# Optimization experiments

Hardware: AMD Instinct MI355X
Metric: run time of the kernel (lower is better)

The kernel has to match this reference:

```python
import jax, jax.numpy as jnp
import numpy as np

D = 512
M_FUT = 3
EPS = 1e-12


def _lin(x, W, b):
    return x @ W + b


def _svd_orthogonalize(m):
    # m: [B, 9] -> [B, 3, 3] SO(3) via SVD orthogonalization (special Procrustes)
    m = m.reshape(-1, 3, 3)
    norm = jnp.maximum(jnp.linalg.norm(m, axis=-1, keepdims=True), EPS)
    mt = jnp.swapaxes(m / norm, -1, -2)          # normalize rows, then transpose
    u, s, vh = jnp.linalg.svd(mt, full_matrices=False)
    v = jnp.swapaxes(vh, -1, -2)                 # torch.svd returns V, jax returns V^H
    ut = jnp.swapaxes(u, -1, -2)
    det = jnp.linalg.det(jnp.matmul(v, ut))      # [B]
    v_adj = jnp.concatenate([v[:, :, :-1], v[:, :, -1:] * det[:, None, None]], axis=2)
    return jnp.matmul(v_adj, ut)


def setup_inputs() -> dict:
    key = jax.random.key(0)
    ks = iter(jax.random.split(key, 40))
    B, N, M = 32, 3, M_FUT
    ph = pw = 37
    BN, hw = B * N, ph * pw
    sc = 1.0 / np.sqrt(D)
    rn = lambda *shape: (jax.random.normal(next(ks), shape, dtype=jnp.float32) * sc)
    inp = {
        'feat': jax.random.normal(next(ks), (BN, hw, D), dtype=jnp.float32),
        'patch_h': ph, 'patch_w': pw, 'batch_size': B, 'num_current_frames': N,
        # two ResConvBlocks, three 512x512 Linears each (in==out -> skip is identity)
        'W_res': rn(2, 3, D, D), 'b_res': rn(2, 3, D),
        # TemporalCameraMLP
        'W_cur1': rn(D, D), 'b_cur1': rn(D), 'W_cur2': rn(D, D), 'b_cur2': rn(D),
        'W_tp1': rn(D, D), 'b_tp1': rn(D), 'W_tp2': rn(D, D * M), 'b_tp2': rn(D * M),
        'W_fut1': rn(D, D), 'b_fut1': rn(D), 'W_fut2': rn(D, D), 'b_fut2': rn(D),
        # more_mlps
        'W_m1': rn(D, D), 'b_m1': rn(D), 'W_m2': rn(D, D), 'b_m2': rn(D),
        # pose heads (fp32)
        'W_t': rn(D, 3), 'b_t': rn(3), 'W_r': rn(D, 9), 'b_r': rn(9),
    }
    return inp


def reference(feat, patch_h, patch_w, batch_size, num_current_frames,
              W_res, b_res, W_cur1, b_cur1, W_cur2, b_cur2,
              W_tp1, b_tp1, W_tp2, b_tp2, W_fut1, b_fut1, W_fut2, b_fut2,
              W_m1, b_m1, W_m2, b_m2, W_t, b_t, W_r, b_r):
    B, N = batch_size, num_current_frames
    M = W_tp2.shape[1] // W_tp2.shape[0]
    # stacked residual 1x1-conv (Linear) blocks
    for i in range(2):
        x = jax.nn.relu(_lin(feat, W_res[i, 0], b_res[i, 0]))
        x = jax.nn.relu(_lin(x, W_res[i, 1], b_res[i, 1]))
        x = jax.nn.relu(_lin(x, W_res[i, 2], b_res[i, 2]))
        feat = feat + x
    # AdaptiveAvgPool2d(1) over patch grid == mean over hw
    pooled = feat.mean(axis=1)                                  # [BN, D]
    # TemporalCameraMLP
    cur = _lin(jax.nn.relu(_lin(pooled, W_cur1, b_cur1)), W_cur2, b_cur2)   # [BN, D]
    gctx = pooled.reshape(B, N, -1).mean(axis=1)                            # [B, D]
    tf = _lin(jax.nn.relu(_lin(gctx, W_tp1, b_tp1)), W_tp2, b_tp2)          # [B, D*M]
    tf = tf.reshape(B * M, -1)
    fut = _lin(jax.nn.relu(_lin(tf, W_fut1, b_fut1)), W_fut2, b_fut2)       # [B*M, D]
    allf = jnp.concatenate([cur, fut], axis=0)                              # [B*(N+M), D]
    h = jax.nn.relu(_lin(jax.nn.relu(_lin(allf, W_m1, b_m1)), W_m2, b_m2))
    # pose head in fp32
    hf = h.astype(jnp.float32)
    out_t = _lin(hf, W_t, b_t)                                  # [newBN, 3]
    out_r = _lin(hf, W_r, b_r)                                  # [newBN, 9]
    r = _svd_orthogonalize(out_r)                               # [newBN, 3, 3]
    newBN = allf.shape[0]
    pose = jnp.zeros((newBN, 4, 4), dtype=jnp.float32)
    pose = pose.at[:, :3, :3].set(r)
    pose = pose.at[:, :3, 3].set(out_t)
    pose = pose.at[:, 3, 3].set(1.0)
    return pose
```

## Files before the change

### kernel.cpp

```cpp
#include <hip/hip_runtime.h>


typedef unsigned short u16;
typedef __attribute__((ext_vector_type(8))) short short8;
typedef __attribute__((ext_vector_type(4))) float f32x4;

constexpr int  DDIM   = 512;
constexpr long R_ROWS = 96L * 1369L;
constexpr long R_PAD  = 1027L * 128L;

__device__ __forceinline__ u16 f2b(float f) {
  union { float f; unsigned u; } x; x.f = f;
  unsigned r = (x.u + 0x7FFFu + ((x.u >> 16) & 1u)) >> 16;
  return (u16)r;
}
__device__ __forceinline__ float b2f(u16 b) {
  union { unsigned u; float f; } x; x.u = ((unsigned)b) << 16;
  return x.f;
}

__global__ void convert_feat_k(const float* __restrict__ in, u16* __restrict__ out) {
  long i4 = ((long)blockIdx.x * 256 + threadIdx.x) * 4;
  if (i4 >= R_PAD * DDIM) return;
  ushort4 o;
  if (i4 < R_ROWS * DDIM) {
    float4 v = *(const float4*)(in + i4);
    o.x = f2b(v.x); o.y = f2b(v.y); o.z = f2b(v.z); o.w = f2b(v.w);
  } else {
    o.x = 0; o.y = 0; o.z = 0; o.w = 0;
  }
  *(ushort4*)(out + i4) = o;
}

__global__ void transpose_w_k(const float* __restrict__ W, u16* __restrict__ Wt) {
  int idx = blockIdx.x * 256 + threadIdx.x;
  if (idx >= 6 * 512 * 512) return;
  int g = idx >> 18, rem = idx & 262143;
  int n = rem >> 9, k = rem & 511;
  Wt[idx] = f2b(W[(long)g * 262144 + (long)k * 512 + n]);
}

template <int MODE>
__global__ __launch_bounds__(256, 2)
void gemm_k(const u16* __restrict__ X, const u16* __restrict__ Wt,
            const float* __restrict__ bias, const u16* Res, u16* Y) {
  __shared__ u16 lA[128 * 64];
  __shared__ u16 lB[128 * 64];
  const int tid  = threadIdx.x;
  const int lane = tid & 63;
  const int wv   = tid >> 6;
  const int wm   = wv & 1;
  const int wn   = wv >> 1;
  const int l15  = lane & 15;
  const int quad = lane >> 4;
  const int colBase = blockIdx.x * 128;
  const long rowBase = (long)blockIdx.y * 128;

  f32x4 acc[4][4];
#pragma unroll
  for (int i = 0; i < 4; ++i)
#pragma unroll
    for (int j = 0; j < 4; ++j) acc[i][j] = (f32x4){0.f, 0.f, 0.f, 0.f};

  for (int k0 = 0; k0 < 512; k0 += 64) {
#pragma unroll
    for (int j = 0; j < 4; ++j) {
      int chunk = tid + 256 * j;
      int r = chunk >> 3, c = chunk & 7;
      const u16* ga = X + (rowBase + r) * DDIM + (k0 + c * 8);
      __builtin_amdgcn_global_load_lds(
          (const __attribute__((address_space(1))) void*)ga,
          (__attribute__((address_space(3))) void*)&lA[chunk * 8], 16, 0, 0);
      const u16* gb = Wt + (long)(colBase + r) * DDIM + (k0 + c * 8);
      __builtin_amdgcn_global_load_lds(
          (const __attribute__((address_space(1))) void*)gb,
          (__attribute__((address_space(3))) void*)&lB[chunk * 8], 16, 0, 0);
    }
    __syncthreads();
#pragma unroll
    for (int kk = 0; kk < 2; ++kk) {
      short8 af[4], bf[4];
#pragma unroll
      for (int i = 0; i < 4; ++i)
        af[i] = *(const short8*)&lA[(wm * 64 + i * 16 + l15) * 64 + kk * 32 + quad * 8];
#pragma unroll
      for (int j = 0; j < 4; ++j)
        bf[j] = *(const short8*)&lB[(wn * 64 + j * 16 + l15) * 64 + kk * 32 + quad * 8];
#pragma unroll
      for (int i = 0; i < 4; ++i)
#pragma unroll
        for (int j = 0; j < 4; ++j)
          acc[i][j] = __builtin_amdgcn_mfma_f32_16x16x32_bf16(af[i], bf[j], acc[i][j], 0, 0, 0);
    }
    __syncthreads();
  }

#pragma unroll
  for (int j = 0; j < 4; ++j) {
    int col = colBase + wn * 64 + j * 16 + l15;
    float bv = bias[col];
#pragma unroll
    for (int i = 0; i < 4; ++i) {
      long row0 = rowBase + wm * 64 + i * 16 + quad * 4;
#pragma unroll
      for (int r = 0; r < 4; ++r) {
        float v = acc[i][j][r] + bv;
        v = fmaxf(v, 0.f);
        long idx = (row0 + r) * DDIM + col;
        if (MODE == 1) v += b2f(Res[idx]);
        Y[idx] = f2b(v);
      }
    }
  }
}

__global__ void zero_k(float* p, int n) {
  int i = blockIdx.x * 256 + threadIdx.x;
  if (i < n) p[i] = 0.f;
}

__global__ void pool_k(const u16* __restrict__ feat, float* __restrict__ pooled) {
  int bn = blockIdx.x, ch = blockIdx.y, d = threadIdx.x;
  int p0 = ch * 172, p1 = p0 + 172;
  if (p1 > 1369) p1 = 1369;
  float s = 0.f;
  long base = ((long)bn * 1369 + p0) * DDIM + d;
  for (int p = p0; p < p1; ++p) { s += b2f(feat[base]); base += DDIM; }
  atomicAdd(&pooled[bn * DDIM + d], s * (1.0f / 1369.0f));
}

__global__ void gctx_k(const float* __restrict__ pooled, float* __restrict__ gctx) {
  int i = blockIdx.x * 256 + threadIdx.x;
  if (i >= 32 * DDIM) return;
  int b = i >> 9, d = i & 511;
  const float* p = pooled + (long)b * 3 * DDIM + d;
  gctx[i] = (p[0] + p[DDIM] + p[2 * DDIM]) * (1.0f / 3.0f);
}

template <bool RELU>
__global__ void lin_k(const float* __restrict__ in, const float* __restrict__ W,
                      const float* __restrict__ bias, float* __restrict__ out,
                      int K, int N) {
  int n = blockIdx.x * 256 + threadIdx.x;
  int r = blockIdx.y;
  if (n >= N) return;
  float acc = bias[n];
  const float* xi = in + (long)r * K;
#pragma unroll 8
  for (int k = 0; k < K; ++k) acc = fmaf(xi[k], W[(long)k * N + n], acc);
  if (RELU) acc = fmaxf(acc, 0.f);
  out[(long)r * N + n] = acc;
}

__global__ void pose_k(const float* __restrict__ h,
                       const float* __restrict__ Wt, const float* __restrict__ bt,
                       const float* __restrict__ Wr, const float* __restrict__ br,
                       float* __restrict__ out) {
  int row = blockIdx.x;
  int lane = threadIdx.x;
  const float* hr = h + (long)row * DDIM;
  float part[12];
#pragma unroll
  for (int c = 0; c < 12; ++c) {
    float acc = 0.f;
    for (int k = lane; k < DDIM; k += 64) {
      float wvv = (c < 3) ? Wt[k * 3 + c] : Wr[k * 9 + (c - 3)];
      acc += hr[k] * wvv;
    }
#pragma unroll
    for (int off = 32; off > 0; off >>= 1) acc += __shfl_down(acc, off);
    part[c] = acc;
  }
  if (lane != 0) return;

  double t3[3];
  for (int i = 0; i < 3; ++i) t3[i] = (double)part[i] + (double)bt[i];
  double m[3][3];
  for (int i = 0; i < 3; ++i)
    for (int j = 0; j < 3; ++j) m[i][j] = (double)part[3 + i * 3 + j] + (double)br[i * 3 + j];
  for (int i = 0; i < 3; ++i) {
    double nn = sqrt(m[i][0] * m[i][0] + m[i][1] * m[i][1] + m[i][2] * m[i][2]);
    if (nn < 1e-12) nn = 1e-12;
    m[i][0] /= nn; m[i][1] /= nn; m[i][2] /= nn;
  }
  double Km[3][3];
  for (int a = 0; a < 3; ++a)
    for (int b = 0; b < 3; ++b) {
      double s = 0;
      for (int i = 0; i < 3; ++i) s += m[i][a] * m[i][b];
      Km[a][b] = s;
    }
  double V[3][3] = {{1, 0, 0}, {0, 1, 0}, {0, 0, 1}};
  const int PQ[3][2] = {{0, 1}, {0, 2}, {1, 2}};
  for (int sweep = 0; sweep < 20; ++sweep) {
    for (int e = 0; e < 3; ++e) {
      int p = PQ[e][0], q = PQ[e][1];
      double apq = Km[p][q];
      if (apq == 0.0) continue;
      double tau = (Km[q][q] - Km[p][p]) / (2.0 * apq);
      double tt = (tau >= 0.0 ? 1.0 : -1.0) / (fabs(tau) + sqrt(1.0 + tau * tau));
      double cc = 1.0 / sqrt(1.0 + tt * tt), ss = tt * cc;
      for (int k = 0; k < 3; ++k) { double a1 = Km[p][k], a2 = Km[q][k]; Km[p][k] = cc * a1 - ss * a2; Km[q][k] = ss * a1 + cc * a2; }
      for (int k = 0; k < 3; ++k) { double a1 = Km[k][p], a2 = Km[k][q]; Km[k][p] = cc * a1 - ss * a2; Km[k][q] = ss * a1 + cc * a2; }
      for (int k = 0; k < 3; ++k) { double a1 = V[k][p], a2 = V[k][q]; V[k][p] = cc * a1 - ss * a2; V[k][q] = ss * a1 + cc * a2; }
    }
  }
  double lam[3] = {Km[0][0], Km[1][1], Km[2][2]};
  int o0 = 0, o1 = 1, o2 = 2; double detV = 1.0;
  if (lam[o0] < lam[o1]) { int t = o0; o0 = o1; o1 = t; detV = -detV; }
  if (lam[o1] < lam[o2]) { int t = o1; o1 = o2; o2 = t; detV = -detV; }
  if (lam[o0] < lam[o1]) { int t = o0; o0 = o1; o1 = t; detV = -detV; }
  double v0[3] = {V[0][o0], V[1][o0], V[2][o0]};
  double v1[3] = {V[0][o1], V[1][o1], V[2][o1]};
  double v2[3] = {V[0][o2], V[1][o2], V[2][o2]};
  double u0[3], u1[3];
  for (int i = 0; i < 3; ++i) u0[i] = m[i][0] * v0[0] + m[i][1] * v0[1] + m[i][2] * v0[2];
  double n0 = sqrt(u0[0] * u0[0] + u0[1] * u0[1] + u0[2] * u0[2]); if (n0 < 1e-30) n0 = 1e-30;
  for (int i = 0; i < 3; ++i) u0[i] /= n0;
  for (int i = 0; i < 3; ++i) u1[i] = m[i][0] * v1[0] + m[i][1] * v1[1] + m[i][2] * v1[2];
  double d01 = u0[0] * u1[0] + u0[1] * u1[1] + u0[2] * u1[2];
  for (int i = 0; i < 3; ++i) u1[i] -= d01 * u0[i];
  double n1 = sqrt(u1[0] * u1[0] + u1[1] * u1[1] + u1[2] * u1[2]); if (n1 < 1e-30) n1 = 1e-30;
  for (int i = 0; i < 3; ++i) u1[i] /= n1;
  double u2[3] = {u0[1] * u1[2] - u0[2] * u1[1],
                  u0[2] * u1[0] - u0[0] * u1[2],
                  u0[0] * u1[1] - u0[1] * u1[0]};
  float* o = out + (long)row * 16;
  for (int i = 0; i < 3; ++i) {
    for (int j = 0; j < 3; ++j)
      o[i * 4 + j] = (float)(u0[i] * v0[j] + u1[i] * v1[j] + detV * u2[i] * v2[j]);
    o[i * 4 + 3] = (float)t3[i];
  }
  o[12] = 0.f; o[13] = 0.f; o[14] = 0.f; o[15] = 1.f;
}

extern "C" void kernel_launch(void* const* d_in, const int* in_sizes, int n_in,
                              void* d_out, int out_size, void* d_ws, size_t ws_size,
                              hipStream_t stream) {
  (void)in_sizes; (void)n_in; (void)out_size; (void)ws_size;
  const float* feat   = (const float*)d_in[0];
  const float* W_res  = (const float*)d_in[5];
  const float* b_res  = (const float*)d_in[6];
  const float* W_cur1 = (const float*)d_in[7];
  const float* b_cur1 = (const float*)d_in[8];
  const float* W_cur2 = (const float*)d_in[9];
  const float* b_cur2 = (const float*)d_in[10];
  const float* W_tp1  = (const float*)d_in[11];
  const float* b_tp1  = (const float*)d_in[12];
  const float* W_tp2  = (const float*)d_in[13];
  const float* b_tp2  = (const float*)d_in[14];
  const float* W_fut1 = (const float*)d_in[15];
  const float* b_fut1 = (const float*)d_in[16];
  const float* W_fut2 = (const float*)d_in[17];
  const float* b_fut2 = (const float*)d_in[18];
  const float* W_m1   = (const float*)d_in[19];
  const float* b_m1   = (const float*)d_in[20];
  const float* W_m2   = (const float*)d_in[21];
  const float* b_m2   = (const float*)d_in[22];
  const float* W_t    = (const float*)d_in[23];
  const float* b_t    = (const float*)d_in[24];
  const float* W_r    = (const float*)d_in[25];
  const float* b_r    = (const float*)d_in[26];

  char* ws = (char*)d_ws;
  const size_t SZ_BIG = (size_t)R_PAD * DDIM * 2;
  u16* A   = (u16*)(ws);
  u16* Bb  = (u16*)(ws + SZ_BIG);
  u16* Cb  = (u16*)(ws + 2 * SZ_BIG);
  u16* Wt6 = (u16*)(ws + 3 * SZ_BIG);
  char* tail = ws + 3 * SZ_BIG + (size_t)6 * 512 * 512 * 2;
  float* pooled = (float*)(tail);
  float* gctx   = pooled + 96 * 512;
  float* tmp    = gctx + 32 * 512;
  float* tfb    = tmp + 192 * 512;
  float* allf   = tfb + 32 * 1536;
  float* h2     = allf + 192 * 512;
  float* outp   = (float*)d_out;

  convert_feat_k<<<65728, 256, 0, stream>>>(feat, A);
  transpose_w_k<<<6144, 256, 0, stream>>>(W_res, Wt6);

  dim3 gg(4, 1027);
  const size_t WS1 = (size_t)512 * 512;
  gemm_k<0><<<gg, 256, 0, stream>>>(A,  Wt6 + 0 * WS1, b_res + 0 * 512, nullptr, Bb);
  gemm_k<0><<<gg, 256, 0, stream>>>(Bb, Wt6 + 1 * WS1, b_res + 1 * 512, nullptr, Cb);
  gemm_k<1><<<gg, 256, 0, stream>>>(Cb, Wt6 + 2 * WS1, b_res + 2 * 512, A, A);
  gemm_k<0><<<gg, 256, 0, stream>>>(A,  Wt6 + 3 * WS1, b_res + 3 * 512, nullptr, Bb);
  gemm_k<0><<<gg, 256, 0, stream>>>(Bb, Wt6 + 4 * WS1, b_res + 4 * 512, nullptr, Cb);
  gemm_k<1><<<gg, 256, 0, stream>>>(Cb, Wt6 + 5 * WS1, b_res + 5 * 512, A, A);

  zero_k<<<(96 * 512 + 255) / 256, 256, 0, stream>>>(pooled, 96 * 512);
  pool_k<<<dim3(96, 8), 512, 0, stream>>>(A, pooled);
  gctx_k<<<(32 * 512 + 255) / 256, 256, 0, stream>>>(pooled, gctx);

  lin_k<true ><<<dim3(2, 96),  256, 0, stream>>>(pooled, W_cur1, b_cur1, tmp, 512, 512);
  lin_k<false><<<dim3(2, 96),  256, 0, stream>>>(tmp, W_cur2, b_cur2, allf, 512, 512);
  lin_k<true ><<<dim3(2, 32),  256, 0, stream>>>(gctx, W_tp1, b_tp1, tmp, 512, 512);
  lin_k<false><<<dim3(6, 32),  256, 0, stream>>>(tmp, W_tp2, b_tp2, tfb, 512, 1536);
  lin_k<true ><<<dim3(2, 96),  256, 0, stream>>>(tfb, W_fut1, b_fut1, tmp, 512, 512);
  lin_k<false><<<dim3(2, 96),  256, 0, stream>>>(tmp, W_fut2, b_fut2, allf + 96 * 512, 512, 512);
  lin_k<true ><<<dim3(2, 192), 256, 0, stream>>>(allf, W_m1, b_m1, tmp, 512, 512);
  lin_k<true ><<<dim3(2, 192), 256, 0, stream>>>(tmp, W_m2, b_m2, h2, 512, 512);

  pose_k<<<192, 64, 0, stream>>>(h2, W_t, b_t, W_r, b_r, outp);
}
```

Before: 1.695 ms.

## Swizzle LDS tiles, group GEMM blocks by row window, raise occupancy

The GEMM kernel now stores A and B tiles in LDS with an XOR swizzle on the 16-byte chunk index. Reads apply the matching swizzle, which is meant to remove bank conflicts on the short8 fragment loads. The 2D grid becomes a 1D grid in which 8 row tiles × 4 column tiles are grouped together, so blocks running at the same time share A rows and weight columns in L2. Launch bounds go from 2 to 4 blocks per CU, which adds some padded blocks that exit early and puts pressure on the register budget.

```diff
diff --git a/kernel.cpp b/kernel.cpp
--- a/kernel.cpp
+++ b/kernel.cpp
@@ -5,9 +5,10 @@
 typedef __attribute__((ext_vector_type(8))) short short8;
 typedef __attribute__((ext_vector_type(4))) float f32x4;
 
-constexpr int  DDIM   = 512;
-constexpr long R_ROWS = 96L * 1369L;
-constexpr long R_PAD  = 1027L * 128L;
+constexpr int  DDIM    = 512;
+constexpr long R_ROWS  = 96L * 1369L;
+constexpr long R_PAD   = 1027L * 128L;
+constexpr int  RT_GRID = 1032;
 
 __device__ __forceinline__ u16 f2b(float f) {
   union { float f; unsigned u; } x; x.f = f;
@@ -41,7 +42,7 @@
 }
 
 template <int MODE>
-__global__ __launch_bounds__(256, 2)
+__global__ __launch_bounds__(256, 4)
 void gemm_k(const u16* __restrict__ X, const u16* __restrict__ Wt,
             const float* __restrict__ bias, const u16* Res, u16* Y) {
   __shared__ u16 lA[128 * 64];
@@ -53,8 +54,14 @@
   const int wn   = wv >> 1;
   const int l15  = lane & 15;
   const int quad = lane >> 4;
-  const int colBase = blockIdx.x * 128;
-  const long rowBase = (long)blockIdx.y * 128;
+
+  const int b   = blockIdx.x;
+  const int win = b >> 5, i32 = b & 31;
+  const int rt  = win * 8 + (i32 & 7);
+  const int ct  = i32 >> 3;
+  if (rt >= 1027) return;
+  const int  colBase = ct * 128;
+  const long rowBase = (long)rt * 128;
 
   f32x4 acc[4][4];
 #pragma unroll
@@ -65,32 +72,34 @@
   for (int k0 = 0; k0 < 512; k0 += 64) {
 #pragma unroll
     for (int j = 0; j < 4; ++j) {
-      int chunk = tid + 256 * j;
-      int r = chunk >> 3, c = chunk & 7;
+      int L = tid + 256 * j;
+      int r = L >> 3, cS = L & 7;
+      int c = cS ^ (r & 7);
       const u16* ga = X + (rowBase + r) * DDIM + (k0 + c * 8);
       __builtin_amdgcn_global_load_lds(
           (const __attribute__((address_space(1))) void*)ga,
-          (__attribute__((address_space(3))) void*)&lA[chunk * 8], 16, 0, 0);
+          (__attribute__((address_space(3))) void*)&lA[L * 8], 16, 0, 0);
       const u16* gb = Wt + (long)(colBase + r) * DDIM + (k0 + c * 8);
       __builtin_amdgcn_global_load_lds(
           (const __attribute__((address_space(1))) void*)gb,
-          (__attribute__((address_space(3))) void*)&lB[chunk * 8], 16, 0, 0);
+          (__attribute__((address_space(3))) void*)&lB[L * 8], 16, 0, 0);
     }
     __syncthreads();
 #pragma unroll
     for (int kk = 0; kk < 2; ++kk) {
-      short8 af[4], bf[4];
+      const int cx = (((kk * 4 + quad) ^ (l15 & 7))) * 8;
+      short8 af[4], bfr[4];
 #pragma unroll
       for (int i = 0; i < 4; ++i)
-        af[i] = *(const short8*)&lA[(wm * 64 + i * 16 + l15) * 64 + kk * 32 + quad * 8];
+        af[i] = *(const short8*)&lA[(wm * 64 + i * 16 + l15) * 64 + cx];
 #pragma unroll
       for (int j = 0; j < 4; ++j)
-        bf[j] = *(const short8*)&lB[(wn * 64 + j * 16 + l15) * 64 + kk * 32 + quad * 8];
+        bfr[j] = *(const short8*)&lB[(wn * 64 + j * 16 + l15) * 64 + cx];
 #pragma unroll
       for (int i = 0; i < 4; ++i)
 #pragma unroll
         for (int j = 0; j < 4; ++j)
-          acc[i][j] = __builtin_amdgcn_mfma_f32_16x16x32_bf16(af[i], bf[j], acc[i][j], 0, 0, 0);
+          acc[i][j] = __builtin_amdgcn_mfma_f32_16x16x32_bf16(af[i], bfr[j], acc[i][j], 0, 0, 0);
     }
     __syncthreads();
   }
@@ -280,14 +289,14 @@
   convert_feat_k<<<65728, 256, 0, stream>>>(feat, A);
   transpose_w_k<<<6144, 256, 0, stream>>>(W_res, Wt6);
 
-  dim3 gg(4, 1027);
+  const int NB = RT_GRID * 4;
   const size_t WS1 = (size_t)512 * 512;
-  gemm_k<0><<<gg, 256, 0, stream>>>(A,  Wt6 + 0 * WS1, b_res + 0 * 512, nullptr, Bb);
-  gemm_k<0><<<gg, 256, 0, stream>>>(Bb, Wt6 + 1 * WS1, b_res + 1 * 512, nullptr, Cb);
-  gemm_k<1><<<gg, 256, 0, stream>>>(Cb, Wt6 + 2 * WS1, b_res + 2 * 512, A, A);
-  gemm_k<0><<<gg, 256, 0, stream>>>(A,  Wt6 + 3 * WS1, b_res + 3 * 512, nullptr, Bb);
-  gemm_k<0><<<gg, 256, 0, stream>>>(Bb, Wt6 + 4 * WS1, b_res + 4 * 512, nullptr, Cb);
-  gemm_k<1><<<gg, 256, 0, stream>>>(Cb, Wt6 + 5 * WS1, b_res + 5 * 512, A, A);
+  gemm_k<0><<<NB, 256, 0, stream>>>(A,  Wt6 + 0 * WS1, b_res + 0 * 512, nullptr, Bb);
+  gemm_k<0><<<NB, 256, 0, stream>>>(Bb, Wt6 + 1 * WS1, b_res + 1 * 512, nullptr, Cb);
+  gemm_k<1><<<NB, 256, 0, stream>>>(Cb, Wt6 + 2 * WS1, b_res + 2 * 512, A, A);
+  gemm_k<0><<<NB, 256, 0, stream>>>(A,  Wt6 + 3 * WS1, b_res + 3 * 512, nullptr, Bb);
+  gemm_k<0><<<NB, 256, 0, stream>>>(Bb, Wt6 + 4 * WS1, b_res + 4 * 512, nullptr, Cb);
+  gemm_k<1><<<NB, 256, 0, stream>>>(Cb, Wt6 + 5 * WS1, b_res + 5 * 512, A, A);
 
   zero_k<<<(96 * 512 + 255) / 256, 256, 0, stream>>>(pooled, 96 * 512);
   pool_k<<<dim3(96, 8), 512, 0, stream>>>(A, pooled);
```

After: 1.634 ms. 3.6% less time.

## Fuse each three-layer residual block into one kernel with LDS-resident activations

Applied to the files above, without the earlier changes.

Replaces six separate 128x128-tiled GEMM launches with two fused kernels. Each kernel keeps a 64-row activation tile (64x512 bf16) in XOR-swizzled LDS across all three linears of a residual block. Weights are prepacked into an MFMA-friendly layout and read directly from global/L2 into registers, and the kernel uses 32x32x16 MFMAs. This removes the intermediate activation round-trips to HBM and the extra buffers. The cost is 64KB of LDS per block, which limits occupancy, and weights are re-read from L2 by every row tile.

```diff
diff --git a/kernel.cpp b/kernel.cpp
--- a/kernel.cpp
+++ b/kernel.cpp
@@ -3,11 +3,11 @@
 
 typedef unsigned short u16;
 typedef __attribute__((ext_vector_type(8))) short short8;
-typedef __attribute__((ext_vector_type(4))) float f32x4;
+typedef __attribute__((ext_vector_type(16))) float f32x16;
 
 constexpr int  DDIM   = 512;
 constexpr long R_ROWS = 96L * 1369L;
-constexpr long R_PAD  = 1027L * 128L;
+constexpr long R_PAD  = 2054L * 64L;
 
 __device__ __forceinline__ u16 f2b(float f) {
   union { float f; unsigned u; } x; x.f = f;
@@ -32,83 +32,115 @@
   *(ushort4*)(out + i4) = o;
 }
 
-__global__ void transpose_w_k(const float* __restrict__ W, u16* __restrict__ Wt) {
-  int idx = blockIdx.x * 256 + threadIdx.x;
-  if (idx >= 6 * 512 * 512) return;
-  int g = idx >> 18, rem = idx & 262143;
-  int n = rem >> 9, k = rem & 511;
-  Wt[idx] = f2b(W[(long)g * 262144 + (long)k * 512 + n]);
-}
-
-template <int MODE>
+__global__ void pack_w_k(const float* __restrict__ W, u16* __restrict__ Wp) {
+  int tid = blockIdx.x * 256 + threadIdx.x;
+  if (tid >= 6 * 262144) return;
+  int g  = tid >> 18, t2 = tid & 262143;
+  int ks = t2 >> 13, t3 = t2 & 8191;
+  int q  = t3 >> 12, t4 = t3 & 4095;
+  int n  = t4 >> 3,  j  = t4 & 7;
+  int k  = ks * 16 + q * 8 + j;
+  Wp[tid] = f2b(W[(long)g * 262144 + (long)k * 512 + n]);
+}
+
 __global__ __launch_bounds__(256, 2)
-void gemm_k(const u16* __restrict__ X, const u16* __restrict__ Wt,
-            const float* __restrict__ bias, const u16* Res, u16* Y) {
-  __shared__ u16 lA[128 * 64];
-  __shared__ u16 lB[128 * 64];
-  const int tid  = threadIdx.x;
+void fused_res_k(u16* __restrict__ Xg, const u16* __restrict__ Wp,
+                 const float* __restrict__ bres) {
+  __shared__ u16 Yb[64 * 512];
+  const int tid = threadIdx.x;
   const int lane = tid & 63;
-  const int wv   = tid >> 6;
-  const int wm   = wv & 1;
-  const int wn   = wv >> 1;
-  const int l15  = lane & 15;
-  const int quad = lane >> 4;
-  const int colBase = blockIdx.x * 128;
-  const long rowBase = (long)blockIdx.y * 128;
-
-  f32x4 acc[4][4];
-#pragma unroll
-  for (int i = 0; i < 4; ++i)
-#pragma unroll
-    for (int j = 0; j < 4; ++j) acc[i][j] = (f32x4){0.f, 0.f, 0.f, 0.f};
-
-  for (int k0 = 0; k0 < 512; k0 += 64) {
-#pragma unroll
-    for (int j = 0; j < 4; ++j) {
-      int chunk = tid + 256 * j;
-      int r = chunk >> 3, c = chunk & 7;
-      const u16* ga = X + (rowBase + r) * DDIM + (k0 + c * 8);
-      __builtin_amdgcn_global_load_lds(
-          (const __attribute__((address_space(1))) void*)ga,
-          (__attribute__((address_space(3))) void*)&lA[chunk * 8], 16, 0, 0);
-      const u16* gb = Wt + (long)(colBase + r) * DDIM + (k0 + c * 8);
-      __builtin_amdgcn_global_load_lds(
-          (const __attribute__((address_space(1))) void*)gb,
-          (__attribute__((address_space(3))) void*)&lB[chunk * 8], 16, 0, 0);
+  const int wvC  = tid >> 6;
+  const int l31  = lane & 31;
+  const int q    = lane >> 5;
+  const long rowBase = (long)blockIdx.x * 64;
+
+#pragma unroll
+  for (int i = 0; i < 16; ++i) {
+    int L = i * 256 + tid;
+    int r = L >> 6, cS = L & 63;
+    int c = cS ^ r;
+    const u16* ga = Xg + (rowBase + r) * DDIM + c * 8;
+    __builtin_amdgcn_global_load_lds(
+        (const __attribute__((address_space(1))) void*)ga,
+        (__attribute__((address_space(3))) void*)&Yb[L * 8], 16, 0, 0);
+  }
+  __syncthreads();
+
+  for (int l = 0; l < 3; ++l) {
+    const u16* wl = Wp + (long)l * 262144;
+    const float* bias = bres + l * 512;
+
+    f32x16 acc[4][2];
+#pragma unroll
+    for (int mi = 0; mi < 4; ++mi)
+#pragma unroll
+      for (int nb = 0; nb < 2; ++nb)
+#pragma unroll
+        for (int e = 0; e < 16; ++e) acc[mi][nb][e] = 0.f;
+
+#pragma unroll 4
+    for (int ks = 0; ks < 32; ++ks) {
+      const int k8 = ks * 2 + q;
+      const u16* wk = wl + ((long)(k8) * 512 + wvC * 128 + l31) * 8;
+      short8 wf[4];
+#pragma unroll
+      for (int mi = 0; mi < 4; ++mi)
+        wf[mi] = *(const short8*)(wk + mi * 32 * 8);
+      short8 xf[2];
+#pragma unroll
+      for (int nb = 0; nb < 2; ++nb) {
+        int r = nb * 32 + l31;
+        xf[nb] = *(const short8*)&Yb[(r * 64 + (k8 ^ r)) * 8];
+      }
+#pragma unroll
+      for (int mi = 0; mi < 4; ++mi)
+#pragma unroll
+        for (int nb = 0; nb < 2; ++nb)
+          acc[mi][nb] = __builtin_amdgcn_mfma_f32_32x32x16_bf16(
+              wf[mi], xf[nb], acc[mi][nb], 0, 0, 0);
     }
     __syncthreads();
-#pragma unroll
-    for (int kk = 0; kk < 2; ++kk) {
-      short8 af[4], bf[4];
-#pragma unroll
-      for (int i = 0; i < 4; ++i)
-        af[i] = *(const short8*)&lA[(wm * 64 + i * 16 + l15) * 64 + kk * 32 + quad * 8];
-#pragma unroll
-      for (int j = 0; j < 4; ++j)
-        bf[j] = *(const short8*)&lB[(wn * 64 + j * 16 + l15) * 64 + kk * 32 + quad * 8];
-#pragma unroll
-      for (int i = 0; i < 4; ++i)
-#pragma unroll
-        for (int j = 0; j < 4; ++j)
-          acc[i][j] = __builtin_amdgcn_mfma_f32_16x16x32_bf16(af[i], bf[j], acc[i][j], 0, 0, 0);
-    }
-    __syncthreads();
-  }
-
-#pragma unroll
-  for (int j = 0; j < 4; ++j) {
-    int col = colBase + wn * 64 + j * 16 + l15;
-    float bv = bias[col];
-#pragma unroll
-    for (int i = 0; i < 4; ++i) {
-      long row0 = rowBase + wm * 64 + i * 16 + quad * 4;
-#pragma unroll
-      for (int r = 0; r < 4; ++r) {
-        float v = acc[i][j][r] + bv;
-        v = fmaxf(v, 0.f);
-        long idx = (row0 + r) * DDIM + col;
-        if (MODE == 1) v += b2f(Res[idx]);
-        Y[idx] = f2b(v);
+
+    if (l < 2) {
+#pragma unroll
+      for (int mi = 0; mi < 4; ++mi) {
+#pragma unroll
+        for (int j2 = 0; j2 < 4; ++j2) {
+          int n0 = wvC * 128 + mi * 32 + 4 * q + 8 * j2;
+          float4 bv = *(const float4*)(bias + n0);
+#pragma unroll
+          for (int nb = 0; nb < 2; ++nb) {
+            int r = nb * 32 + l31;
+            ushort4 pk;
+            pk.x = f2b(fmaxf(acc[mi][nb][4 * j2 + 0] + bv.x, 0.f));
+            pk.y = f2b(fmaxf(acc[mi][nb][4 * j2 + 1] + bv.y, 0.f));
+            pk.z = f2b(fmaxf(acc[mi][nb][4 * j2 + 2] + bv.z, 0.f));
+            pk.w = f2b(fmaxf(acc[mi][nb][4 * j2 + 3] + bv.w, 0.f));
+            *(ushort4*)&Yb[(r * 64 + ((n0 >> 3) ^ r)) * 8 + (n0 & 7)] = pk;
+          }
+        }
+      }
+      __syncthreads();
+    } else {
+#pragma unroll
+      for (int mi = 0; mi < 4; ++mi) {
+#pragma unroll
+        for (int j2 = 0; j2 < 4; ++j2) {
+          int n0 = wvC * 128 + mi * 32 + 4 * q + 8 * j2;
+          float4 bv = *(const float4*)(bias + n0);
+#pragma unroll
+          for (int nb = 0; nb < 2; ++nb) {
+            int r = nb * 32 + l31;
+            u16* gp = Xg + (rowBase + r) * DDIM + n0;
+            ushort4 xv = *(const ushort4*)gp;
+            ushort4 pk;
+            pk.x = f2b(fmaxf(acc[mi][nb][4 * j2 + 0] + bv.x, 0.f) + b2f(xv.x));
+            pk.y = f2b(fmaxf(acc[mi][nb][4 * j2 + 1] + bv.y, 0.f) + b2f(xv.y));
+            pk.z = f2b(fmaxf(acc[mi][nb][4 * j2 + 2] + bv.z, 0.f) + b2f(xv.z));
+            pk.w = f2b(fmaxf(acc[mi][nb][4 * j2 + 3] + bv.w, 0.f) + b2f(xv.w));
+            *(ushort4*)gp = pk;
+          }
+        }
       }
     }
   }
@@ -194,15 +226,15 @@
   const int PQ[3][2] = {{0, 1}, {0, 2}, {1, 2}};
   for (int sweep = 0; sweep < 20; ++sweep) {
     for (int e = 0; e < 3; ++e) {
-      int p = PQ[e][0], q = PQ[e][1];
-      double apq = Km[p][q];
+      int p = PQ[e][0], qq = PQ[e][1];
+      double apq = Km[p][qq];
       if (apq == 0.0) continue;
-      double tau = (Km[q][q] - Km[p][p]) / (2.0 * apq);
+      double tau = (Km[qq][qq] - Km[p][p]) / (2.0 * apq);
       double tt = (tau >= 0.0 ? 1.0 : -1.0) / (fabs(tau) + sqrt(1.0 + tau * tau));
       double cc = 1.0 / sqrt(1.0 + tt * tt), ss = tt * cc;
-      for (int k = 0; k < 3; ++k) { double a1 = Km[p][k], a2 = Km[q][k]; Km[p][k] = cc * a1 - ss * a2; Km[q][k] = ss * a1 + cc * a2; }
-      for (int k = 0; k < 3; ++k) { double a1 = Km[k][p], a2 = Km[k][q]; Km[k][p] = cc * a1 - ss * a2; Km[k][q] = ss * a1 + cc * a2; }
-      for (int k = 0; k < 3; ++k) { double a1 = V[k][p], a2 = V[k][q]; V[k][p] = cc * a1 - ss * a2; V[k][q] = ss * a1 + cc * a2; }
+      for (int k = 0; k < 3; ++k) { double a1 = Km[p][k], a2 = Km[qq][k]; Km[p][k] = cc * a1 - ss * a2; Km[qq][k] = ss * a1 + cc * a2; }
+      for (int k = 0; k < 3; ++k) { double a1 = Km[k][p], a2 = Km[k][qq]; Km[k][p] = cc * a1 - ss * a2; Km[k][qq] = ss * a1 + cc * a2; }
+      for (int k = 0; k < 3; ++k) { double a1 = V[k][p], a2 = V[k][qq]; V[k][p] = cc * a1 - ss * a2; V[k][qq] = ss * a1 + cc * a2; }
     }
   }
   double lam[3] = {Km[0][0], Km[1][1], Km[2][2]};
@@ -264,11 +296,9 @@
 
   char* ws = (char*)d_ws;
   const size_t SZ_BIG = (size_t)R_PAD * DDIM * 2;
-  u16* A   = (u16*)(ws);
-  u16* Bb  = (u16*)(ws + SZ_BIG);
-  u16* Cb  = (u16*)(ws + 2 * SZ_BIG);
-  u16* Wt6 = (u16*)(ws + 3 * SZ_BIG);
-  char* tail = ws + 3 * SZ_BIG + (size_t)6 * 512 * 512 * 2;
+  u16* A  = (u16*)(ws);
+  u16* Wp = (u16*)(ws + SZ_BIG);
+  char* tail = ws + SZ_BIG + (size_t)6 * 262144 * 2;
   float* pooled = (float*)(tail);
   float* gctx   = pooled + 96 * 512;
   float* tmp    = gctx + 32 * 512;
@@ -278,16 +308,10 @@
   float* outp   = (float*)d_out;
 
   convert_feat_k<<<65728, 256, 0, stream>>>(feat, A);
-  transpose_w_k<<<6144, 256, 0, stream>>>(W_res, Wt6);
-
-  dim3 gg(4, 1027);
-  const size_t WS1 = (size_t)512 * 512;
-  gemm_k<0><<<gg, 256, 0, stream>>>(A,  Wt6 + 0 * WS1, b_res + 0 * 512, nullptr, Bb);
-  gemm_k<0><<<gg, 256, 0, stream>>>(Bb, Wt6 + 1 * WS1, b_res + 1 * 512, nullptr, Cb);
-  gemm_k<1><<<gg, 256, 0, stream>>>(Cb, Wt6 + 2 * WS1, b_res + 2 * 512, A, A);
-  gemm_k<0><<<gg, 256, 0, stream>>>(A,  Wt6 + 3 * WS1, b_res + 3 * 512, nullptr, Bb);
-  gemm_k<0><<<gg, 256, 0, stream>>>(Bb, Wt6 + 4 * WS1, b_res + 4 * 512, nullptr, Cb);
-  gemm_k<1><<<gg, 256, 0, stream>>>(Cb, Wt6 + 5 * WS1, b_res + 5 * 512, A, A);
+  pack_w_k<<<6144, 256, 0, stream>>>(W_res, Wp);
+
+  fused_res_k<<<2054, 256, 0, stream>>>(A, Wp,                 b_res);
+  fused_res_k<<<2054, 256, 0, stream>>>(A, Wp + 3L * 262144,   b_res + 3 * 512);
 
   zero_k<<<(96 * 512 + 255) / 256, 256, 0, stream>>>(pooled, 96 * 512);
   pool_k<<<dim3(96, 8), 512, 0, stream>>>(A, pooled);
```

New measurement: 1.675 ms. About the same (-1.2%).
